# Kernel tuning notes

Measured on AMD Instinct MI355X. Metric: run time of the kernel, lower is better.

The kernel has to match this reference:

```python
import jax, jax.numpy as jnp
import numpy as np

HEADS = 4

def setup_inputs() -> dict:
    B, L, D = 4, 2048, 256
    key = jax.random.key(0)
    k1, k2, k3, k4, k5, k6 = jax.random.split(key, 6)
    return {
        "atten": jax.random.normal(k1, (B, L, L), dtype=jnp.float32),
        "value": jax.random.normal(k2, (B, L, D), dtype=jnp.float32),
        "mask": jax.random.uniform(k3, (B, 1, L, L), dtype=jnp.float32),
        "padding_mask": jax.random.randint(k4, (B, L, L), 0, 2, dtype=jnp.int32),
        "Wv": jax.random.normal(k5, (D, D), dtype=jnp.float32) * 0.02,
        "bv": jnp.zeros((D,), dtype=jnp.float32),
        "Wo": jax.random.normal(k6, (D, D), dtype=jnp.float32) * 0.02,
        "bo": jnp.zeros((D,), dtype=jnp.float32),
    }

def reference(atten, value, mask, padding_mask, Wv, bv, Wo, bo):
    B, L, D = value.shape
    H = HEADS
    dk = D // H
    # to_value: Linear then split heads. N == 1 (value.unsqueeze(1) in torch).
    v = value @ Wv + bv                                   # (B, L, D)
    v = v.reshape(B, 1, L, H, dk).transpose(0, 3, 1, 2, 4)  # (B, H, N=1, L, dk)
    # externally supplied attention logits, two sequential masked fills
    a = atten[:, None, :, :]                              # (B, 1, L, L)
    a = jnp.where(mask < 0.5, jnp.finfo(a.dtype).min, a)
    a = jnp.where(padding_mask[:, None, :, :] == 0, -jnp.inf, a)
    a = jax.nn.softmax(a, axis=-1)                        # (B, 1, L, L)
    # dropout is identity in eval mode
    # einsum 'bhij,bhnjk->bhnik' with h=1 on a broadcast across H heads of v
    out = jnp.einsum('bij,bhnjk->bhnik', a[:, 0], v)      # (B, H, 1, L, dk)
    out = out.transpose(0, 2, 3, 1, 4).reshape(B, 1, L, D)
    out = out @ Wo + bo                                   # (B, 1, L, D)
    return out
```

## Files before the change

kernel.cpp:

```cpp
#include <hip/hip_runtime.h>
#include <hip/hip_bf16.h>
#include <math.h>

#define L 2048
#define D 256
#define NEG_FLT_MAX (-3.402823466e38f)

typedef __attribute__((ext_vector_type(8))) short bf16x8;
typedef __attribute__((ext_vector_type(4))) float f32x4;
typedef __attribute__((ext_vector_type(4))) int i32x4;

__device__ __forceinline__ unsigned short f2bf(float f) {
    union { float f; unsigned int u; } v; v.f = f;
    unsigned int r = v.u + 0x7FFFu + ((v.u >> 16) & 1u);
    return (unsigned short)(r >> 16);
}

__global__ __launch_bounds__(256) void wtrans_kernel(
    const float* __restrict__ Wv, const float* __restrict__ Wo,
    unsigned short* __restrict__ Wvt, unsigned short* __restrict__ Wot) {
    int idx = blockIdx.x * 256 + threadIdx.x;
    int which = idx >> 16;
    int e = idx & 65535;
    int k = e >> 8, n = e & 255;
    const float* W = which ? Wo : Wv;
    unsigned short* Wt = which ? Wot : Wvt;
    Wt[n * 256 + k] = f2bf(W[k * 256 + n]);
}

__global__ __launch_bounds__(256) void gemm_v_kernel(
    const float* __restrict__ A,
    const unsigned short* __restrict__ Wt,
    const float* __restrict__ bias,
    unsigned short* __restrict__ Vt) {
    const int wave = threadIdx.x >> 6;
    const int lane = threadIdx.x & 63;
    const int lm = lane & 15, q = lane >> 4;
    const int rh = wave >> 1;
    const int nh = wave & 1;
    const int m0 = blockIdx.x * 32;
    const int n0 = blockIdx.y * 64;
    const int arow = m0 + rh * 16 + lm;

    int ncol[2];
#pragma unroll
    for (int nf = 0; nf < 2; nf++) ncol[nf] = n0 + nh * 32 + nf * 16 + lm;

    f32x4 acc[2];
    acc[0] = (f32x4)(0.f); acc[1] = (f32x4)(0.f);

    const float* ap = A + (size_t)arow * 256;
    f32x4 pa0 = *reinterpret_cast<const f32x4*>(ap + q * 8);
    f32x4 pa1 = *reinterpret_cast<const f32x4*>(ap + q * 8 + 4);
    bf16x8 pb0 = *reinterpret_cast<const bf16x8*>(Wt + (size_t)ncol[0] * 256 + q * 8);
    bf16x8 pb1 = *reinterpret_cast<const bf16x8*>(Wt + (size_t)ncol[1] * 256 + q * 8);

    for (int k0 = 0; k0 < 256; k0 += 32) {
        f32x4 a0 = pa0, a1 = pa1;
        bf16x8 b0 = pb0, b1 = pb1;
        if (k0 < 224) {
            int kq = k0 + 32 + q * 8;
            pa0 = *reinterpret_cast<const f32x4*>(ap + kq);
            pa1 = *reinterpret_cast<const f32x4*>(ap + kq + 4);
            pb0 = *reinterpret_cast<const bf16x8*>(Wt + (size_t)ncol[0] * 256 + kq);
            pb1 = *reinterpret_cast<const bf16x8*>(Wt + (size_t)ncol[1] * 256 + kq);
        }
        bf16x8 afr;
#pragma unroll
        for (int e = 0; e < 4; e++) afr[e] = (short)f2bf(a0[e]);
#pragma unroll
        for (int e = 0; e < 4; e++) afr[4 + e] = (short)f2bf(a1[e]);
        acc[0] = __builtin_amdgcn_mfma_f32_16x16x32_bf16(afr, b0, acc[0], 0, 0, 0);
        acc[1] = __builtin_amdgcn_mfma_f32_16x16x32_bf16(afr, b1, acc[1], 0, 0, 0);
    }

    int mrow = m0 + rh * 16 + q * 4;
    int b = mrow >> 11;
    int j = mrow & 2047;
#pragma unroll
    for (int nf = 0; nf < 2; nf++) {
        int n = ncol[nf];
        float bias_n = bias[n];
        unsigned short* dst = Vt + (size_t)b * (D * L) + (size_t)n * L + j;
        ushort4 pk;
        pk.x = f2bf(acc[nf][0] + bias_n);
        pk.y = f2bf(acc[nf][1] + bias_n);
        pk.z = f2bf(acc[nf][2] + bias_n);
        pk.w = f2bf(acc[nf][3] + bias_n);
        *reinterpret_cast<ushort4*>(dst) = pk;
    }
}

__global__ __launch_bounds__(512, 4) void attn_kernel(
    const float* __restrict__ atten, const float* __restrict__ mask,
    const int* __restrict__ pad, const unsigned short* __restrict__ Vt,
    const unsigned short* __restrict__ Wot, const float* __restrict__ bo,
    float* __restrict__ out) {
    const int g = blockIdx.x;
    const int b = g >> 7;
    const int i0 = (g & 127) * 16;
    const int tid = threadIdx.x;
    const int wave = tid >> 6, lane = tid & 63;
    const int lm = lane & 15, q = lane >> 4;
    const int kg = wave >> 2;
    const int ng = wave & 3;
    const int r = tid >> 5;
    const int c = (tid & 31) * 4;

    __shared__ __align__(16) unsigned short Plds[2][16][136];
    __shared__ __align__(16) float acc_lds[16][264];
    __shared__ __align__(16) unsigned short A_lds[16][264];
    __shared__ float l_lds[16];

    f32x4 acc[4];
#pragma unroll
    for (int nf = 0; nf < 4; nf++) acc[nf] = (f32x4)(0.f);
    float lsum = 0.f;

    const size_t rowoff = ((size_t)(b * L + i0 + r)) * L + c;
    const float* at_row = atten + rowoff;
    const float* mk_row = mask + rowoff;
    const int* pd_row = pad + rowoff;
    const unsigned short* vt_b = Vt + (size_t)b * (D * L);

    f32x4 na = *reinterpret_cast<const f32x4*>(at_row);
    f32x4 nk = *reinterpret_cast<const f32x4*>(mk_row);
    i32x4 np = *reinterpret_cast<const i32x4*>(pd_row);

    for (int jt = 0; jt < 16; jt++) {
        const int j0 = jt * 128;
        bf16x8 bfr[2][4];
#pragma unroll
        for (int kk = 0; kk < 2; kk++)
#pragma unroll
            for (int nf = 0; nf < 4; nf++) {
                int n = ng * 64 + nf * 16 + lm;
                bfr[kk][nf] = *reinterpret_cast<const bf16x8*>(
                    vt_b + (size_t)n * L + j0 + kg * 64 + kk * 32 + q * 8);
            }
        f32x4 a = na, k = nk;
        i32x4 p = np;
        if (jt < 15) {
            na = *reinterpret_cast<const f32x4*>(at_row + j0 + 128);
            nk = *reinterpret_cast<const f32x4*>(mk_row + j0 + 128);
            np = *reinterpret_cast<const i32x4*>(pd_row + j0 + 128);
        }
        ushort4 pk;
        float pe[4];
#pragma unroll
        for (int e = 0; e < 4; e++) {
            float sv = (k[e] < 0.5f) ? NEG_FLT_MAX : a[e];
            sv = (p[e] == 0) ? -INFINITY : sv;
            pe[e] = __expf(sv);
        }
        lsum += (pe[0] + pe[1]) + (pe[2] + pe[3]);
        pk.x = f2bf(pe[0]); pk.y = f2bf(pe[1]);
        pk.z = f2bf(pe[2]); pk.w = f2bf(pe[3]);

        const int par = jt & 1;
        *reinterpret_cast<ushort4*>(&Plds[par][r][c]) = pk;
        __syncthreads();

#pragma unroll
        for (int kk = 0; kk < 2; kk++) {
            bf16x8 afr = *reinterpret_cast<const bf16x8*>(
                &Plds[par][lm][kg * 64 + kk * 32 + q * 8]);
#pragma unroll
            for (int nf = 0; nf < 4; nf++)
                acc[nf] = __builtin_amdgcn_mfma_f32_16x16x32_bf16(
                    afr, bfr[kk][nf], acc[nf], 0, 0, 0);
        }
    }

#pragma unroll
    for (int off = 1; off < 32; off <<= 1) lsum += __shfl_xor(lsum, off);
    if ((tid & 31) == 0) l_lds[r] = lsum;

    if (kg == 1) {
#pragma unroll
        for (int nf = 0; nf < 4; nf++) {
            int n = ng * 64 + nf * 16 + lm;
#pragma unroll
            for (int rg = 0; rg < 4; rg++)
                acc_lds[q * 4 + rg][n] = acc[nf][rg];
        }
    }
    __syncthreads();

    if (kg == 0) {
#pragma unroll
        for (int nf = 0; nf < 4; nf++) {
            int n = ng * 64 + nf * 16 + lm;
#pragma unroll
            for (int rg = 0; rg < 4; rg++) {
                int rr = q * 4 + rg;
                float tot = acc[nf][rg] + acc_lds[rr][n];
                A_lds[rr][n] = f2bf(tot / l_lds[rr]);
            }
        }
    }
    __syncthreads();

    f32x4 oacc[2];
    oacc[0] = (f32x4)(0.f); oacc[1] = (f32x4)(0.f);
    for (int k0 = 0; k0 < 256; k0 += 32) {
        bf16x8 afr = *reinterpret_cast<const bf16x8*>(&A_lds[lm][k0 + q * 8]);
#pragma unroll
        for (int nf = 0; nf < 2; nf++) {
            int n = wave * 32 + nf * 16 + lm;
            bf16x8 bfr = *reinterpret_cast<const bf16x8*>(
                Wot + (size_t)n * 256 + k0 + q * 8);
            oacc[nf] = __builtin_amdgcn_mfma_f32_16x16x32_bf16(
                afr, bfr, oacc[nf], 0, 0, 0);
        }
    }
#pragma unroll
    for (int nf = 0; nf < 2; nf++) {
        int n = wave * 32 + nf * 16 + lm;
        float bias_n = bo[n];
#pragma unroll
        for (int rg = 0; rg < 4; rg++)
            out[((size_t)(b * L + i0 + q * 4 + rg)) * 256 + n] = oacc[nf][rg] + bias_n;
    }
}

extern "C" void kernel_launch(void* const* d_in, const int* in_sizes, int n_in,
                              void* d_out, int out_size, void* d_ws, size_t ws_size,
                              hipStream_t stream) {
    (void)in_sizes; (void)n_in; (void)out_size; (void)ws_size;
    const float* atten = (const float*)d_in[0];
    const float* value = (const float*)d_in[1];
    const float* mask  = (const float*)d_in[2];
    const int*   pad   = (const int*)d_in[3];
    const float* Wv    = (const float*)d_in[4];
    const float* bv    = (const float*)d_in[5];
    const float* Wo    = (const float*)d_in[6];
    const float* bo    = (const float*)d_in[7];
    float* out = (float*)d_out;

    char* ws = (char*)d_ws;
    unsigned short* Vt  = (unsigned short*)(ws);
    unsigned short* Wvt = (unsigned short*)(ws + 4194304);
    unsigned short* Wot = (unsigned short*)(ws + 4325376);

    wtrans_kernel<<<512, 256, 0, stream>>>(Wv, Wo, Wvt, Wot);
    gemm_v_kernel<<<dim3(256, 4), 256, 0, stream>>>(value, Wvt, bv, Vt);
    attn_kernel<<<512, 512, 0, stream>>>(atten, mask, pad, Vt, Wot, bo, out);
}
```

Measured before the change: 261.2 us.

## Build softmax P fragments in registers instead of staging through LDS

Each wave now loads atten, mask and padding directly in the MFMA A-fragment layout and computes exp and the bf16 conversion into its own registers. This removes the per-tile shared-memory staging of P and the __syncthreads on every tile. The row sums are reduced with two shuffles and two partial arrays that are combined at the end, and the acc_lds padding is changed. In exchange, the four waves sharing a k-group redundantly load and exponentiate the same inputs (four times the load and exp instructions), and each lane's global reads are less coalesced.

```diff
diff --git a/kernel.cpp b/kernel.cpp
--- a/kernel.cpp
+++ b/kernel.cpp
@@ -104,28 +104,31 @@
     const int lm = lane & 15, q = lane >> 4;
     const int kg = wave >> 2;
     const int ng = wave & 3;
-    const int r = tid >> 5;
-    const int c = (tid & 31) * 4;
-
-    __shared__ __align__(16) unsigned short Plds[2][16][136];
-    __shared__ __align__(16) float acc_lds[16][264];
+
+    __shared__ float acc_lds[16][258];
     __shared__ __align__(16) unsigned short A_lds[16][264];
-    __shared__ float l_lds[16];
+    __shared__ float l_part[2][16];
 
     f32x4 acc[4];
 #pragma unroll
     for (int nf = 0; nf < 4; nf++) acc[nf] = (f32x4)(0.f);
     float lsum = 0.f;
 
-    const size_t rowoff = ((size_t)(b * L + i0 + r)) * L + c;
-    const float* at_row = atten + rowoff;
-    const float* mk_row = mask + rowoff;
-    const int* pd_row = pad + rowoff;
-    const unsigned short* vt_b = Vt + (size_t)b * (D * L);
-
-    f32x4 na = *reinterpret_cast<const f32x4*>(at_row);
-    f32x4 nk = *reinterpret_cast<const f32x4*>(mk_row);
-    i32x4 np = *reinterpret_cast<const i32x4*>(pd_row);
+    const size_t rowoff = ((size_t)(b * L + i0 + lm)) * L + kg * 64 + q * 8;
+    const float* at_p = atten + rowoff;
+    const float* mk_p = mask + rowoff;
+    const int*   pd_p = pad + rowoff;
+    const unsigned short* vt_b = Vt + (size_t)b * (D * L) + kg * 64 + q * 8;
+
+    f32x4 pa[4], pm[4];
+    i32x4 pp[4];
+#pragma unroll
+    for (int u = 0; u < 4; u++) {
+        int off = (u >> 1) * 32 + (u & 1) * 4;
+        pa[u] = *reinterpret_cast<const f32x4*>(at_p + off);
+        pm[u] = *reinterpret_cast<const f32x4*>(mk_p + off);
+        pp[u] = *reinterpret_cast<const i32x4*>(pd_p + off);
+    }
 
     for (int jt = 0; jt < 16; jt++) {
         const int j0 = jt * 128;
@@ -136,45 +139,45 @@
             for (int nf = 0; nf < 4; nf++) {
                 int n = ng * 64 + nf * 16 + lm;
                 bfr[kk][nf] = *reinterpret_cast<const bf16x8*>(
-                    vt_b + (size_t)n * L + j0 + kg * 64 + kk * 32 + q * 8);
-            }
-        f32x4 a = na, k = nk;
-        i32x4 p = np;
+                    vt_b + (size_t)n * L + j0 + kk * 32);
+            }
+        f32x4 ca[4], cm[4];
+        i32x4 cp[4];
+#pragma unroll
+        for (int u = 0; u < 4; u++) { ca[u] = pa[u]; cm[u] = pm[u]; cp[u] = pp[u]; }
         if (jt < 15) {
-            na = *reinterpret_cast<const f32x4*>(at_row + j0 + 128);
-            nk = *reinterpret_cast<const f32x4*>(mk_row + j0 + 128);
-            np = *reinterpret_cast<const i32x4*>(pd_row + j0 + 128);
-        }
-        ushort4 pk;
-        float pe[4];
-#pragma unroll
-        for (int e = 0; e < 4; e++) {
-            float sv = (k[e] < 0.5f) ? NEG_FLT_MAX : a[e];
-            sv = (p[e] == 0) ? -INFINITY : sv;
-            pe[e] = __expf(sv);
-        }
-        lsum += (pe[0] + pe[1]) + (pe[2] + pe[3]);
-        pk.x = f2bf(pe[0]); pk.y = f2bf(pe[1]);
-        pk.z = f2bf(pe[2]); pk.w = f2bf(pe[3]);
-
-        const int par = jt & 1;
-        *reinterpret_cast<ushort4*>(&Plds[par][r][c]) = pk;
-        __syncthreads();
-
-#pragma unroll
-        for (int kk = 0; kk < 2; kk++) {
-            bf16x8 afr = *reinterpret_cast<const bf16x8*>(
-                &Plds[par][lm][kg * 64 + kk * 32 + q * 8]);
+#pragma unroll
+            for (int u = 0; u < 4; u++) {
+                int off = j0 + 128 + (u >> 1) * 32 + (u & 1) * 4;
+                pa[u] = *reinterpret_cast<const f32x4*>(at_p + off);
+                pm[u] = *reinterpret_cast<const f32x4*>(mk_p + off);
+                pp[u] = *reinterpret_cast<const i32x4*>(pd_p + off);
+            }
+        }
+        bf16x8 afr[2];
+#pragma unroll
+        for (int u = 0; u < 4; u++) {
+            int kk = u >> 1, h = u & 1;
+#pragma unroll
+            for (int e = 0; e < 4; e++) {
+                float sv = (cm[u][e] < 0.5f) ? NEG_FLT_MAX : ca[u][e];
+                sv = (cp[u][e] == 0) ? -INFINITY : sv;
+                float pv = __expf(sv);
+                lsum += pv;
+                afr[kk][h * 4 + e] = (short)f2bf(pv);
+            }
+        }
+#pragma unroll
+        for (int kk = 0; kk < 2; kk++)
 #pragma unroll
             for (int nf = 0; nf < 4; nf++)
                 acc[nf] = __builtin_amdgcn_mfma_f32_16x16x32_bf16(
-                    afr, bfr[kk][nf], acc[nf], 0, 0, 0);
-        }
-    }
-
-#pragma unroll
-    for (int off = 1; off < 32; off <<= 1) lsum += __shfl_xor(lsum, off);
-    if ((tid & 31) == 0) l_lds[r] = lsum;
+                    afr[kk], bfr[kk][nf], acc[nf], 0, 0, 0);
+    }
+
+    lsum += __shfl_xor(lsum, 16);
+    lsum += __shfl_xor(lsum, 32);
+    if (ng == 0 && q == 0) l_part[kg][lm] = lsum;
 
     if (kg == 1) {
 #pragma unroll
@@ -195,7 +198,8 @@
             for (int rg = 0; rg < 4; rg++) {
                 int rr = q * 4 + rg;
                 float tot = acc[nf][rg] + acc_lds[rr][n];
-                A_lds[rr][n] = f2bf(tot / l_lds[rr]);
+                float lv = l_part[0][rr] + l_part[1][rr];
+                A_lds[rr][n] = f2bf(tot / lv);
             }
         }
     }
```

After: 328.0 us. 25.6% more time.

## Fuse weight transpose into V GEMM and drop split-K waves in attention kernel

Applied to the files above, without the earlier changes.

The Wv transpose/convert step is folded into the V projection kernel: each block loads its Wv slice into LDS transposed, and the Wo transpose is spread across blocks of the same launch. This removes one kernel launch and the workspace round trip. The attention kernel goes from 512 threads with a two-way split over the key dimension to 256 threads, each wave covering the full key tile. That drops the cross-wave accumulator reduction through LDS, and each thread now loads 8 elements per row chunk. The trade is fewer resident waves to hide memory latency, plus more V-fragment registers per wave. There is also a possible race: prep_kernel writes Wot while attn reads it, but attn runs as a separate later launch, so this is fine.

```diff
diff --git a/kernel.cpp b/kernel.cpp
--- a/kernel.cpp
+++ b/kernel.cpp
@@ -16,55 +16,64 @@
     return (unsigned short)(r >> 16);
 }
 
-__global__ __launch_bounds__(256) void wtrans_kernel(
-    const float* __restrict__ Wv, const float* __restrict__ Wo,
-    unsigned short* __restrict__ Wvt, unsigned short* __restrict__ Wot) {
-    int idx = blockIdx.x * 256 + threadIdx.x;
-    int which = idx >> 16;
-    int e = idx & 65535;
-    int k = e >> 8, n = e & 255;
-    const float* W = which ? Wo : Wv;
-    unsigned short* Wt = which ? Wot : Wvt;
-    Wt[n * 256 + k] = f2bf(W[k * 256 + n]);
-}
-
-__global__ __launch_bounds__(256) void gemm_v_kernel(
-    const float* __restrict__ A,
-    const unsigned short* __restrict__ Wt,
-    const float* __restrict__ bias,
-    unsigned short* __restrict__ Vt) {
-    const int wave = threadIdx.x >> 6;
-    const int lane = threadIdx.x & 63;
+__global__ __launch_bounds__(256, 4) void prep_kernel(
+    const float* __restrict__ value, const float* __restrict__ Wv,
+    const float* __restrict__ bv, const float* __restrict__ Wo,
+    unsigned short* __restrict__ Vt, unsigned short* __restrict__ Wot) {
+    const int tid = threadIdx.x;
+    const int wave = tid >> 6, lane = tid & 63;
     const int lm = lane & 15, q = lane >> 4;
     const int rh = wave >> 1;
     const int nh = wave & 1;
     const int m0 = blockIdx.x * 32;
     const int n0 = blockIdx.y * 64;
+
+    __shared__ __align__(16) unsigned short Wlds[64][264];
+
+    {
+        int bid = blockIdx.y * 256 + blockIdx.x;
+        if (tid < 64) {
+            int e = bid * 64 + tid;
+            int k = e >> 8, n = e & 255;
+            Wot[n * 256 + k] = f2bf(Wo[k * 256 + n]);
+        }
+    }
+
+    {
+        int krow = tid >> 4;
+        int nrel = (tid & 15) * 4;
+#pragma unroll
+        for (int p = 0; p < 16; p++) {
+            int k = p * 16 + krow;
+            f32x4 w = *reinterpret_cast<const f32x4*>(Wv + (size_t)k * 256 + n0 + nrel);
+            Wlds[nrel + 0][k] = f2bf(w[0]);
+            Wlds[nrel + 1][k] = f2bf(w[1]);
+            Wlds[nrel + 2][k] = f2bf(w[2]);
+            Wlds[nrel + 3][k] = f2bf(w[3]);
+        }
+    }
+    __syncthreads();
+
+    const int nl0 = nh * 32 + lm;
+    const int nl1 = nh * 32 + 16 + lm;
     const int arow = m0 + rh * 16 + lm;
-
-    int ncol[2];
-#pragma unroll
-    for (int nf = 0; nf < 2; nf++) ncol[nf] = n0 + nh * 32 + nf * 16 + lm;
 
     f32x4 acc[2];
     acc[0] = (f32x4)(0.f); acc[1] = (f32x4)(0.f);
 
-    const float* ap = A + (size_t)arow * 256;
+    const float* ap = value + (size_t)arow * 256;
     f32x4 pa0 = *reinterpret_cast<const f32x4*>(ap + q * 8);
     f32x4 pa1 = *reinterpret_cast<const f32x4*>(ap + q * 8 + 4);
-    bf16x8 pb0 = *reinterpret_cast<const bf16x8*>(Wt + (size_t)ncol[0] * 256 + q * 8);
-    bf16x8 pb1 = *reinterpret_cast<const bf16x8*>(Wt + (size_t)ncol[1] * 256 + q * 8);
 
     for (int k0 = 0; k0 < 256; k0 += 32) {
         f32x4 a0 = pa0, a1 = pa1;
-        bf16x8 b0 = pb0, b1 = pb1;
         if (k0 < 224) {
             int kq = k0 + 32 + q * 8;
             pa0 = *reinterpret_cast<const f32x4*>(ap + kq);
             pa1 = *reinterpret_cast<const f32x4*>(ap + kq + 4);
-            pb0 = *reinterpret_cast<const bf16x8*>(Wt + (size_t)ncol[0] * 256 + kq);
-            pb1 = *reinterpret_cast<const bf16x8*>(Wt + (size_t)ncol[1] * 256 + kq);
-        }
+        }
+        bf16x8 b0 = *reinterpret_cast<const bf16x8*>(&Wlds[nl0][k0 + q * 8]);
+        bf16x8 b1 = *reinterpret_cast<const bf16x8*>(&Wlds[nl1][k0 + q * 8]);
         bf16x8 afr;
 #pragma unroll
         for (int e = 0; e < 4; e++) afr[e] = (short)f2bf(a0[e]);
@@ -79,19 +88,20 @@
     int j = mrow & 2047;
 #pragma unroll
     for (int nf = 0; nf < 2; nf++) {
-        int n = ncol[nf];
-        float bias_n = bias[n];
+        int n = n0 + nh * 32 + nf * 16 + lm;
+        float bias_n = bv[n];
+        const f32x4& a = acc[nf];
         unsigned short* dst = Vt + (size_t)b * (D * L) + (size_t)n * L + j;
         ushort4 pk;
-        pk.x = f2bf(acc[nf][0] + bias_n);
-        pk.y = f2bf(acc[nf][1] + bias_n);
-        pk.z = f2bf(acc[nf][2] + bias_n);
-        pk.w = f2bf(acc[nf][3] + bias_n);
+        pk.x = f2bf(a[0] + bias_n);
+        pk.y = f2bf(a[1] + bias_n);
+        pk.z = f2bf(a[2] + bias_n);
+        pk.w = f2bf(a[3] + bias_n);
         *reinterpret_cast<ushort4*>(dst) = pk;
     }
 }
 
-__global__ __launch_bounds__(512, 4) void attn_kernel(
+__global__ __launch_bounds__(256, 2) void attn_kernel(
     const float* __restrict__ atten, const float* __restrict__ mask,
     const int* __restrict__ pad, const unsigned short* __restrict__ Vt,
     const unsigned short* __restrict__ Wot, const float* __restrict__ bo,
@@ -102,13 +112,10 @@
     const int tid = threadIdx.x;
     const int wave = tid >> 6, lane = tid & 63;
     const int lm = lane & 15, q = lane >> 4;
-    const int kg = wave >> 2;
-    const int ng = wave & 3;
-    const int r = tid >> 5;
-    const int c = (tid & 31) * 4;
+    const int r = tid >> 4;
+    const int c = (tid & 15) * 8;
 
     __shared__ __align__(16) unsigned short Plds[2][16][136];
-    __shared__ __align__(16) float acc_lds[16][264];
     __shared__ __align__(16) unsigned short A_lds[16][264];
     __shared__ float l_lds[16];
 
@@ -118,53 +125,61 @@
     float lsum = 0.f;
 
     const size_t rowoff = ((size_t)(b * L + i0 + r)) * L + c;
-    const float* at_row = atten + rowoff;
-    const float* mk_row = mask + rowoff;
-    const int* pd_row = pad + rowoff;
+    const float* at_p = atten + rowoff;
+    const float* mk_p = mask + rowoff;
+    const int*   pd_p = pad + rowoff;
     const unsigned short* vt_b = Vt + (size_t)b * (D * L);
 
-    f32x4 na = *reinterpret_cast<const f32x4*>(at_row);
-    f32x4 nk = *reinterpret_cast<const f32x4*>(mk_row);
-    i32x4 np = *reinterpret_cast<const i32x4*>(pd_row);
+    f32x4 pa0 = *reinterpret_cast<const f32x4*>(at_p);
+    f32x4 pa1 = *reinterpret_cast<const f32x4*>(at_p + 4);
+    f32x4 pm0 = *reinterpret_cast<const f32x4*>(mk_p);
+    f32x4 pm1 = *reinterpret_cast<const f32x4*>(mk_p + 4);
+    i32x4 pp0 = *reinterpret_cast<const i32x4*>(pd_p);
+    i32x4 pp1 = *reinterpret_cast<const i32x4*>(pd_p + 4);
 
     for (int jt = 0; jt < 16; jt++) {
         const int j0 = jt * 128;
-        bf16x8 bfr[2][4];
-#pragma unroll
-        for (int kk = 0; kk < 2; kk++)
+        bf16x8 bfr[4][4];
+#pragma unroll
+        for (int kk = 0; kk < 4; kk++)
 #pragma unroll
             for (int nf = 0; nf < 4; nf++) {
-                int n = ng * 64 + nf * 16 + lm;
+                int n = wave * 64 + nf * 16 + lm;
                 bfr[kk][nf] = *reinterpret_cast<const bf16x8*>(
-                    vt_b + (size_t)n * L + j0 + kg * 64 + kk * 32 + q * 8);
+                    vt_b + (size_t)n * L + j0 + kk * 32 + q * 8);
             }
-        f32x4 a = na, k = nk;
-        i32x4 p = np;
+        f32x4 a0 = pa0, a1 = pa1, k0 = pm0, k1 = pm1;
+        i32x4 p0 = pp0, p1 = pp1;
         if (jt < 15) {
-            na = *reinterpret_cast<const f32x4*>(at_row + j0 + 128);
-            nk = *reinterpret_cast<const f32x4*>(mk_row + j0 + 128);
-            np = *reinterpret_cast<const i32x4*>(pd_row + j0 + 128);
-        }
-        ushort4 pk;
-        float pe[4];
+            pa0 = *reinterpret_cast<const f32x4*>(at_p + j0 + 128);
+            pa1 = *reinterpret_cast<const f32x4*>(at_p + j0 + 132);
+            pm0 = *reinterpret_cast<const f32x4*>(mk_p + j0 + 128);
+            pm1 = *reinterpret_cast<const f32x4*>(mk_p + j0 + 132);
+            pp0 = *reinterpret_cast<const i32x4*>(pd_p + j0 + 128);
+            pp1 = *reinterpret_cast<const i32x4*>(pd_p + j0 + 132);
+        }
+        bf16x8 pk;
 #pragma unroll
         for (int e = 0; e < 4; e++) {
-            float sv = (k[e] < 0.5f) ? NEG_FLT_MAX : a[e];
-            sv = (p[e] == 0) ? -INFINITY : sv;
-            pe[e] = __expf(sv);
-        }
-        lsum += (pe[0] + pe[1]) + (pe[2] + pe[3]);
-        pk.x = f2bf(pe[0]); pk.y = f2bf(pe[1]);
-        pk.z = f2bf(pe[2]); pk.w = f2bf(pe[3]);
-
+            float sv = (k0[e] < 0.5f) ? NEG_FLT_MAX : a0[e];
+            sv = (p0[e] == 0) ? -INFINITY : sv;
+            float pv = __expf(sv);
+            lsum += pv;
+            pk[e] = (short)f2bf(pv);
+            float sw = (k1[e] < 0.5f) ? NEG_FLT_MAX : a1[e];
+            sw = (p1[e] == 0) ? -INFINITY : sw;
+            float pw = __expf(sw);
+            lsum += pw;
+            pk[4 + e] = (short)f2bf(pw);
+        }
         const int par = jt & 1;
-        *reinterpret_cast<ushort4*>(&Plds[par][r][c]) = pk;
+        *reinterpret_cast<bf16x8*>(&Plds[par][r][c]) = pk;
         __syncthreads();
 
 #pragma unroll
-        for (int kk = 0; kk < 2; kk++) {
+        for (int kk = 0; kk < 4; kk++) {
             bf16x8 afr = *reinterpret_cast<const bf16x8*>(
-                &Plds[par][lm][kg * 64 + kk * 32 + q * 8]);
+                &Plds[par][lm][kk * 32 + q * 8]);
 #pragma unroll
             for (int nf = 0; nf < 4; nf++)
                 acc[nf] = __builtin_amdgcn_mfma_f32_16x16x32_bf16(
@@ -172,51 +187,42 @@
         }
     }
 
-#pragma unroll
-    for (int off = 1; off < 32; off <<= 1) lsum += __shfl_xor(lsum, off);
-    if ((tid & 31) == 0) l_lds[r] = lsum;
-
-    if (kg == 1) {
-#pragma unroll
-        for (int nf = 0; nf < 4; nf++) {
-            int n = ng * 64 + nf * 16 + lm;
-#pragma unroll
-            for (int rg = 0; rg < 4; rg++)
-                acc_lds[q * 4 + rg][n] = acc[nf][rg];
-        }
-    }
+    lsum += __shfl_xor(lsum, 1);
+    lsum += __shfl_xor(lsum, 2);
+    lsum += __shfl_xor(lsum, 4);
+    lsum += __shfl_xor(lsum, 8);
+    if ((tid & 15) == 0) l_lds[r] = lsum;
     __syncthreads();
 
-    if (kg == 0) {
-#pragma unroll
-        for (int nf = 0; nf < 4; nf++) {
-            int n = ng * 64 + nf * 16 + lm;
-#pragma unroll
-            for (int rg = 0; rg < 4; rg++) {
-                int rr = q * 4 + rg;
-                float tot = acc[nf][rg] + acc_lds[rr][n];
-                A_lds[rr][n] = f2bf(tot / l_lds[rr]);
-            }
-        }
+    float linv[4];
+#pragma unroll
+    for (int rg = 0; rg < 4; rg++) linv[rg] = 1.f / l_lds[q * 4 + rg];
+#pragma unroll
+    for (int nf = 0; nf < 4; nf++) {
+        int n = wave * 64 + nf * 16 + lm;
+#pragma unroll
+        for (int rg = 0; rg < 4; rg++)
+            A_lds[q * 4 + rg][n] = f2bf(acc[nf][rg] * linv[rg]);
     }
     __syncthreads();
 
-    f32x4 oacc[2];
-    oacc[0] = (f32x4)(0.f); oacc[1] = (f32x4)(0.f);
+    f32x4 oacc[4];
+#pragma unroll
+    for (int nf = 0; nf < 4; nf++) oacc[nf] = (f32x4)(0.f);
     for (int k0 = 0; k0 < 256; k0 += 32) {
         bf16x8 afr = *reinterpret_cast<const bf16x8*>(&A_lds[lm][k0 + q * 8]);
 #pragma unroll
-        for (int nf = 0; nf < 2; nf++) {
-            int n = wave * 32 + nf * 16 + lm;
-            bf16x8 bfr = *reinterpret_cast<const bf16x8*>(
+        for (int nf = 0; nf < 4; nf++) {
+            int n = wave * 64 + nf * 16 + lm;
+            bf16x8 bfrW = *reinterpret_cast<const bf16x8*>(
                 Wot + (size_t)n * 256 + k0 + q * 8);
             oacc[nf] = __builtin_amdgcn_mfma_f32_16x16x32_bf16(
-                afr, bfr, oacc[nf], 0, 0, 0);
-        }
-    }
-#pragma unroll
-    for (int nf = 0; nf < 2; nf++) {
-        int n = wave * 32 + nf * 16 + lm;
+                afr, bfrW, oacc[nf], 0, 0, 0);
+        }
+    }
+#pragma unroll
+    for (int nf = 0; nf < 4; nf++) {
+        int n = wave * 64 + nf * 16 + lm;
         float bias_n = bo[n];
 #pragma unroll
         for (int rg = 0; rg < 4; rg++)
@@ -240,10 +246,8 @@
 
     char* ws = (char*)d_ws;
     unsigned short* Vt  = (unsigned short*)(ws);
-    unsigned short* Wvt = (unsigned short*)(ws + 4194304);
-    unsigned short* Wot = (unsigned short*)(ws + 4325376);
-
-    wtrans_kernel<<<512, 256, 0, stream>>>(Wv, Wo, Wvt, Wot);
-    gemm_v_kernel<<<dim3(256, 4), 256, 0, stream>>>(value, Wvt, bv, Vt);
-    attn_kernel<<<512, 512, 0, stream>>>(atten, mask, pad, Vt, Wot, bo, out);
-}
+    unsigned short* Wot = (unsigned short*)(ws + 4194304);
+
+    prep_kernel<<<dim3(256, 4), 256, 0, stream>>>(value, Wv, bv, Wo, Vt, Wot);
+    attn_kernel<<<512, 256, 0, stream>>>(atten, mask, pad, Vt, Wot, bo, out);
+}
```

New measurement: 254.1 us. -2.7%, faster.
